# Kernel optimization log

Measured on AMD Instinct MI355X. Metric: run time of the kernel, lower is better.

Reference implementation:

```python
import jax, jax.numpy as jnp
import numpy as np

HEAD_DIM = 128
NUM_Q_HEADS = 32
NUM_KV_HEADS = 8
ROPE_BASE = 500000.0
# llama3 rope scaling constants
OLD_CTX = 8192.0
SCALE_FACTOR = 8.0
LOW_FREQ_FACTOR = 1.0
HIGH_FREQ_FACTOR = 4.0


def _llama3_inv_freq(dim):
    inv_freq = ROPE_BASE ** (-jnp.arange(0, dim, 2, dtype=jnp.float32) / dim)
    wavelen = 2.0 * jnp.pi / inv_freq
    low_wl = OLD_CTX / LOW_FREQ_FACTOR
    high_wl = OLD_CTX / HIGH_FREQ_FACTOR
    smooth = (OLD_CTX / wavelen - LOW_FREQ_FACTOR) / (HIGH_FREQ_FACTOR - LOW_FREQ_FACTOR)
    smoothed = (1.0 - smooth) * inv_freq / SCALE_FACTOR + smooth * inv_freq
    return jnp.where(wavelen > low_wl, inv_freq / SCALE_FACTOR,
                     jnp.where(wavelen < high_wl, inv_freq, smoothed))


def _apply_rope(x, cos, sin):
    # x: [B,N,H,D]; cos/sin: [B,N,1,D/2]  (NeoX rotate-half convention)
    x1, x2 = jnp.split(x, 2, axis=-1)
    return jnp.concatenate([x1 * cos - x2 * sin, x2 * cos + x1 * sin], axis=-1)


def setup_inputs() -> dict:
    key = jax.random.key(0)
    k1, k2, k3 = jax.random.split(key, 3)
    B, N, H = 2, 2048, 4096
    qkv_out = (NUM_Q_HEADS + 2 * NUM_KV_HEADS) * HEAD_DIM  # 6144
    x = jax.random.normal(k1, (B, N, H), dtype=jnp.float32)
    positions = jnp.tile(jnp.arange(N, dtype=jnp.int32), (B, 1))
    wqkv = jax.random.normal(k2, (H, qkv_out), dtype=jnp.float32) * 0.02
    wo = jax.random.normal(k3, (NUM_Q_HEADS * HEAD_DIM, H), dtype=jnp.float32) * 0.02
    return {"x": x, "positions": positions, "wqkv": wqkv, "wo": wo}


def reference(x, positions, wqkv, wo):
    B, N, H = x.shape
    q_size = NUM_Q_HEADS * HEAD_DIM
    kv_size = NUM_KV_HEADS * HEAD_DIM
    # fused QKV projection
    qkv = jnp.einsum('bnh,hd->bnd', x, wqkv)
    q, k, v = jnp.split(qkv, [q_size, q_size + kv_size], axis=-1)
    q = q.reshape(B, N, NUM_Q_HEADS, HEAD_DIM)
    k = k.reshape(B, N, NUM_KV_HEADS, HEAD_DIM)
    v = v.reshape(B, N, NUM_KV_HEADS, HEAD_DIM)
    # llama3-scaled RoPE
    inv_freq = _llama3_inv_freq(HEAD_DIM)  # [D/2]
    freqs = positions[..., None].astype(jnp.float32) * inv_freq  # [B,N,D/2]
    cos = jnp.cos(freqs)[:, :, None, :]
    sin = jnp.sin(freqs)[:, :, None, :]
    q = _apply_rope(q, cos, sin)
    k = _apply_rope(k, cos, sin)
    # GQA causal attention
    g = NUM_Q_HEADS // NUM_KV_HEADS
    qg = q.reshape(B, N, NUM_KV_HEADS, g, HEAD_DIM)
    scale = 1.0 / np.sqrt(HEAD_DIM).astype(np.float32)
    scores = jnp.einsum('bnkgd,bmkd->bkgnm', qg, k) * scale  # [B,KV,G,N,N]
    causal = jnp.tril(jnp.ones((N, N), dtype=bool))
    scores = jnp.where(causal, scores, jnp.finfo(scores.dtype).min)
    p = jax.nn.softmax(scores, axis=-1)
    o = jnp.einsum('bkgnm,bmkd->bnkgd', p, v).reshape(B, N, NUM_Q_HEADS * HEAD_DIM)
    return jnp.einsum('bnd,dh->bnh', o, wo)
```

## Files before the change

### kernel.cpp

```cpp
#include <hip/hip_runtime.h>
#include <math.h>

typedef float  floatx4 __attribute__((ext_vector_type(4)));
typedef short  shortx8 __attribute__((ext_vector_type(8)));
typedef __bf16 bf16x8  __attribute__((ext_vector_type(8)));

static __device__ __forceinline__ floatx4 mfma16(shortx8 a, shortx8 b, floatx4 c) {
  return __builtin_amdgcn_mfma_f32_16x16x32_bf16(
      __builtin_bit_cast(bf16x8, a), __builtin_bit_cast(bf16x8, b), c, 0, 0, 0);
}
static __device__ __forceinline__ unsigned short f2bf(float f) {
  unsigned int u = __builtin_bit_cast(unsigned int, f);
  u += 0x7fffu + ((u >> 16) & 1u);
  return (unsigned short)(u >> 16);
}
static __device__ __forceinline__ float bf2f(unsigned short h) {
  unsigned int u = ((unsigned int)h) << 16;
  return __builtin_bit_cast(float, u);
}
static __device__ __forceinline__ unsigned int packbf2(float lo, float hi) {
  return (unsigned int)f2bf(lo) | ((unsigned int)f2bf(hi) << 16);
}

#define GLOAD_LDS16(gp, lp) \
  __builtin_amdgcn_global_load_lds((const __attribute__((address_space(1))) void*)(gp), \
                                   (__attribute__((address_space(3))) void*)(lp), 16, 0, 0)

__global__ __launch_bounds__(256) void conv_kernel(const float* __restrict__ in,
                                                   unsigned short* __restrict__ out, long n4) {
  long i = (long)blockIdx.x * 256 + threadIdx.x;
  if (i < n4) {
    float4 v = ((const float4*)in)[i];
    uint2 st;
    st.x = packbf2(v.x, v.y);
    st.y = packbf2(v.z, v.w);
    ((uint2*)out)[i] = st;
  }
}

__global__ __launch_bounds__(256) void tconv_kernel(const float* __restrict__ in,
                                                    unsigned short* __restrict__ out,
                                                    int R, int C) {
  __shared__ float t[32][33];
  const int r0 = blockIdx.x * 32, c0 = blockIdx.y * 32;
  const int tr = threadIdx.x >> 3, tq = threadIdx.x & 7;
  float4 v = *(const float4*)(in + (long)(r0 + tr) * C + c0 + tq * 4);
  t[tr][tq * 4 + 0] = v.x;
  t[tr][tq * 4 + 1] = v.y;
  t[tr][tq * 4 + 2] = v.z;
  t[tr][tq * 4 + 3] = v.w;
  __syncthreads();
  const int cl = tr, rq = tq;
  uint2 st;
  st.x = packbf2(t[rq * 4 + 0][cl], t[rq * 4 + 1][cl]);
  st.y = packbf2(t[rq * 4 + 2][cl], t[rq * 4 + 3][cl]);
  *(uint2*)(out + (long)(c0 + cl) * R + r0 + rq * 4) = st;
}

template<int C_BF16>
__global__ __launch_bounds__(256) void gemm_tt(const unsigned short* __restrict__ A,
                                               const unsigned short* __restrict__ BT,
                                               void* __restrict__ Cp,
                                               int Nn, int K, int lda) {
  __shared__ alignas(16) short As[128 * 32];
  __shared__ alignas(16) short Bs[128 * 32];
  const int tid = threadIdx.x;
  const int lane = tid & 63, w = tid >> 6;
  const int l15 = lane & 15, lg = lane >> 4;
  const int wr = w >> 1, wc = w & 1;
  const int klg = lg ^ ((l15 >> 1) & 3);
  const long m0 = (long)blockIdx.x * 128;
  const long n0 = (long)blockIdx.y * 128;

  floatx4 acc[4][4];
#pragma unroll
  for (int m = 0; m < 4; ++m)
#pragma unroll
    for (int n = 0; n < 4; ++n) acc[m][n] = (floatx4)0.0f;

  for (int k0 = 0; k0 < K; k0 += 32) {
#pragma unroll
    for (int i = 0; i < 2; ++i) {
      int c = i * 256 + tid;
      int row = c >> 2, j = c & 3;
      int kc = j ^ ((row >> 1) & 3);
      const unsigned short* ga = A + (m0 + row) * (long)lda + k0 + kc * 8;
      GLOAD_LDS16(ga, (char*)As + i * 4096 + w * 1024);
      const unsigned short* gb = BT + (n0 + row) * (long)K + k0 + kc * 8;
      GLOAD_LDS16(gb, (char*)Bs + i * 4096 + w * 1024);
    }
    __syncthreads();

    shortx8 afr[4], bfr[4];
#pragma unroll
    for (int m = 0; m < 4; ++m)
      afr[m] = *(const shortx8*)((char*)As + (wr * 64 + m * 16 + l15) * 64 + klg * 16);
#pragma unroll
    for (int n = 0; n < 4; ++n)
      bfr[n] = *(const shortx8*)((char*)Bs + (wc * 64 + n * 16 + l15) * 64 + klg * 16);
#pragma unroll
    for (int m = 0; m < 4; ++m)
#pragma unroll
      for (int n = 0; n < 4; ++n)
        acc[m][n] = mfma16(afr[m], bfr[n], acc[m][n]);
    __syncthreads();
  }

#pragma unroll
  for (int m = 0; m < 4; ++m)
#pragma unroll
    for (int n = 0; n < 4; ++n)
#pragma unroll
      for (int r = 0; r < 4; ++r) {
        long row = m0 + wr * 64 + m * 16 + lg * 4 + r;
        long col = n0 + wc * 64 + n * 16 + l15;
        float val = acc[m][n][r];
        if constexpr (C_BF16) ((unsigned short*)Cp)[row * Nn + col] = f2bf(val);
        else                  ((float*)Cp)[row * Nn + col] = val;
      }
}

template<int A_BF16, int C_BF16>
__global__ __launch_bounds__(256) void gemm_fb(const void* __restrict__ Ap,
                                               const float* __restrict__ Bp,
                                               void* __restrict__ Cp,
                                               int M, int Nn, int K, int lda) {
  __shared__ alignas(16) short As[128 * 40];
  __shared__ alignas(16) short Bs[128 * 40];
  const int tid = threadIdx.x;
  const int lane = tid & 63, w = tid >> 6;
  const int l15 = lane & 15, lg = lane >> 4;
  const int wr = w >> 1, wc = w & 1;
  const long m0 = (long)blockIdx.x * 128;
  const long n0 = (long)blockIdx.y * 128;

  floatx4 acc[4][4];
#pragma unroll
  for (int m = 0; m < 4; ++m)
#pragma unroll
    for (int n = 0; n < 4; ++n) acc[m][n] = (floatx4)0.0f;

  for (int k0 = 0; k0 < K; k0 += 32) {
    if constexpr (A_BF16) {
      const unsigned short* A = (const unsigned short*)Ap;
#pragma unroll
      for (int i = 0; i < 2; ++i) {
        int qi = tid + 256 * i;
        int row = qi >> 2, ch = qi & 3;
        uint4 v = *(const uint4*)(A + (m0 + row) * (long)lda + k0 + ch * 8);
        *(uint4*)((char*)As + row * 80 + ch * 16) = v;
      }
    } else {
      const float* A = (const float*)Ap;
#pragma unroll
      for (int i = 0; i < 4; ++i) {
        int qi = tid + 256 * i;
        int row = qi >> 3, q = qi & 7;
        float4 v = *(const float4*)(A + (m0 + row) * (long)lda + k0 + q * 4);
        uint2 st;
        st.x = packbf2(v.x, v.y);
        st.y = packbf2(v.z, v.w);
        *(uint2*)((char*)As + row * 80 + q * 8) = st;
      }
    }
#pragma unroll
    for (int i = 0; i < 2; ++i) {
      int qi = tid + 256 * i;
      int kp = qi >> 5, q = qi & 31;
      const float* B0 = Bp + (long)(k0 + 2 * kp) * Nn + n0 + q * 4;
      float4 a = *(const float4*)B0;
      float4 b = *(const float4*)(B0 + Nn);
      const float* af_ = (const float*)&a;
      const float* bf_ = (const float*)&b;
#pragma unroll
      for (int j = 0; j < 4; ++j) {
        int col = q * 4 + j;
        *(unsigned int*)((char*)Bs + col * 80 + kp * 4) = packbf2(af_[j], bf_[j]);
      }
    }
    __syncthreads();

    shortx8 afr[4], bfr[4];
#pragma unroll
    for (int m = 0; m < 4; ++m)
      afr[m] = *(const shortx8*)((char*)As + (wr * 64 + m * 16 + l15) * 80 + lg * 16);
#pragma unroll
    for (int n = 0; n < 4; ++n)
      bfr[n] = *(const shortx8*)((char*)Bs + (wc * 64 + n * 16 + l15) * 80 + lg * 16);
#pragma unroll
    for (int m = 0; m < 4; ++m)
#pragma unroll
      for (int n = 0; n < 4; ++n)
        acc[m][n] = mfma16(afr[m], bfr[n], acc[m][n]);
    __syncthreads();
  }

#pragma unroll
  for (int m = 0; m < 4; ++m)
#pragma unroll
    for (int n = 0; n < 4; ++n)
#pragma unroll
      for (int r = 0; r < 4; ++r) {
        long row = m0 + wr * 64 + m * 16 + lg * 4 + r;
        long col = n0 + wc * 64 + n * 16 + l15;
        float val = acc[m][n][r];
        if constexpr (C_BF16) ((unsigned short*)Cp)[row * Nn + col] = f2bf(val);
        else                  ((float*)Cp)[row * Nn + col] = val;
      }
}

__global__ __launch_bounds__(256) void rope_kernel(unsigned short* __restrict__ qkv,
                                                   const int* __restrict__ pos) {
  const int token = blockIdx.x;
  const int tid = threadIdx.x;
  __shared__ float cs[64], sn[64];
  if (tid < 64) {
    float d = (float)tid;
    float inv = powf(500000.0f, -d * (1.0f / 64.0f));
    float wl = 6.283185307179586f / inv;
    float scaled;
    if (wl > 8192.0f) scaled = inv * 0.125f;
    else if (wl < 2048.0f) scaled = inv;
    else {
      float smooth = (8192.0f / wl - 1.0f) * (1.0f / 3.0f);
      scaled = (1.0f - smooth) * inv * 0.125f + smooth * inv;
    }
    float ang = (float)pos[token] * scaled;
    cs[tid] = cosf(ang);
    sn[tid] = sinf(ang);
  }
  __syncthreads();
  const long base = (long)token * 6144;
#pragma unroll
  for (int it = 0; it < 10; ++it) {
    int p = tid + 256 * it;
    int h = p >> 6, d = p & 63;
    long i0 = base + h * 128 + d;
    float a = bf2f(qkv[i0]);
    float b = bf2f(qkv[i0 + 64]);
    float c = cs[d], s = sn[d];
    qkv[i0]      = f2bf(a * c - b * s);
    qkv[i0 + 64] = f2bf(b * c + a * s);
  }
}

#define SCALE_QK 0.08838834764831845f
__global__ __launch_bounds__(256) void attn_kernel(unsigned short* __restrict__ qkv) {
  const int tid = threadIdx.x;
  const int w = tid >> 6, lane = tid & 63;
  const int l15 = lane & 15, lg = lane >> 4;
  const int qblk = blockIdx.x, qh = blockIdx.y, b = blockIdx.z;
  const int kvh = qh >> 2;
  const int q0 = qblk * 64;
  const long rowbase = (long)b * 2048;

  __shared__ alignas(16) short Ks[64 * 128];
  __shared__ alignas(16) short Vt[128 * 64];
  __shared__ alignas(16) short Ps[4][16 * 64];

  shortx8 qf[4];
  {
    long qrow = rowbase + q0 + w * 16 + l15;
    const unsigned short* qp = qkv + qrow * 6144 + qh * 128 + lg * 8;
#pragma unroll
    for (int dc = 0; dc < 4; ++dc) qf[dc] = *(const shortx8*)(qp + dc * 32);
  }

  floatx4 accO[8];
#pragma unroll
  for (int i = 0; i < 8; ++i) accO[i] = (floatx4)0.0f;
  float m_r[4], l_r[4];
#pragma unroll
  for (int r = 0; r < 4; ++r) { m_r[r] = -INFINITY; l_r[r] = 0.0f; }

  const int nt = qblk + 1;
  for (int t = 0; t < nt; ++t) {
    const int kt0 = t * 64;
#pragma unroll
    for (int i = 0; i < 4; ++i) {
      int ci = tid + 256 * i;
      int tok = ci >> 4, ch = ci & 15;
      uint4 v = *(const uint4*)(qkv + (rowbase + kt0 + tok) * 6144 + 4096 + kvh * 128 + ch * 8);
      int byte = (tok * 256 + ch * 16) ^ ((tok & 7) << 4);
      *(uint4*)((char*)Ks + byte) = v;
    }
#pragma unroll
    for (int i = 0; i < 4; ++i) {
      int ci = tid + 256 * i;
      int tok = ci >> 4, ch = ci & 15;
      uint4 v = *(const uint4*)(qkv + (rowbase + kt0 + tok) * 6144 + 5120 + kvh * 128 + ch * 8);
      const unsigned short* e = (const unsigned short*)&v;
#pragma unroll
      for (int j = 0; j < 8; ++j) {
        int d = ch * 8 + j;
        int byte = (d * 128 + tok * 2) ^ (((d ^ (d >> 3)) & 7) << 4);
        *(short*)((char*)Vt + byte) = (short)e[j];
      }
    }
    __syncthreads();

    floatx4 accS[4];
#pragma unroll
    for (int c = 0; c < 4; ++c) accS[c] = (floatx4)0.0f;
#pragma unroll
    for (int c = 0; c < 4; ++c) {
      int tok = c * 16 + l15;
      int rb = tok * 256, sw = (tok & 7) << 4;
#pragma unroll
      for (int dc = 0; dc < 4; ++dc) {
        shortx8 kf = *(const shortx8*)((char*)Ks + ((rb + dc * 64 + lg * 16) ^ sw));
        accS[c] = mfma16(qf[dc], kf, accS[c]);
      }
    }

    float sv[4][4], rm[4];
    const int growb = q0 + w * 16 + lg * 4;
    const bool diag = (t == nt - 1);
#pragma unroll
    for (int r = 0; r < 4; ++r) rm[r] = -INFINITY;
#pragma unroll
    for (int c = 0; c < 4; ++c) {
      int gcol = kt0 + c * 16 + l15;
#pragma unroll
      for (int r = 0; r < 4; ++r) {
        float s = accS[c][r] * SCALE_QK;
        if (diag && gcol > growb + r) s = -1e30f;
        sv[c][r] = s;
        rm[r] = fmaxf(rm[r], s);
      }
    }
#pragma unroll
    for (int r = 0; r < 4; ++r) {
      rm[r] = fmaxf(rm[r], __shfl_xor(rm[r], 1));
      rm[r] = fmaxf(rm[r], __shfl_xor(rm[r], 2));
      rm[r] = fmaxf(rm[r], __shfl_xor(rm[r], 4));
      rm[r] = fmaxf(rm[r], __shfl_xor(rm[r], 8));
    }
    float alpha[4], rs[4], mn[4];
#pragma unroll
    for (int r = 0; r < 4; ++r) {
      mn[r] = fmaxf(m_r[r], rm[r]);
      alpha[r] = __expf(m_r[r] - mn[r]);
      rs[r] = 0.0f;
    }
    char* Pw = (char*)&Ps[w][0];
#pragma unroll
    for (int c = 0; c < 4; ++c) {
#pragma unroll
      for (int r = 0; r < 4; ++r) {
        float p = __expf(sv[c][r] - mn[r]);
        rs[r] += p;
        int row = lg * 4 + r, col = c * 16 + l15;
        int byte = (row * 128 + col * 2) ^ ((row & 7) << 4);
        *(short*)(Pw + byte) = (short)f2bf(p);
      }
    }
#pragma unroll
    for (int r = 0; r < 4; ++r) {
      rs[r] += __shfl_xor(rs[r], 1);
      rs[r] += __shfl_xor(rs[r], 2);
      rs[r] += __shfl_xor(rs[r], 4);
      rs[r] += __shfl_xor(rs[r], 8);
      l_r[r] = l_r[r] * alpha[r] + rs[r];
      m_r[r] = mn[r];
    }
#pragma unroll
    for (int db = 0; db < 8; ++db)
#pragma unroll
      for (int r = 0; r < 4; ++r) accO[db][r] *= alpha[r];

#pragma unroll
    for (int kc = 0; kc < 2; ++kc) {
      int pb = (l15 * 128 + kc * 64 + lg * 16) ^ ((l15 & 7) << 4);
      shortx8 pf = *(const shortx8*)(Pw + pb);
#pragma unroll
      for (int db = 0; db < 8; ++db) {
        int d = db * 16 + l15;
        int vb = (d * 128 + kc * 64 + lg * 16) ^ (((d ^ (d >> 3)) & 7) << 4);
        shortx8 vf = *(const shortx8*)((char*)Vt + vb);
        accO[db] = mfma16(pf, vf, accO[db]);
      }
    }
    __syncthreads();
  }

  {
    long orow_base = rowbase + q0 + w * 16 + lg * 4;
#pragma unroll
    for (int r = 0; r < 4; ++r) {
      float inv_l = 1.0f / l_r[r];
      unsigned short* op = qkv + (orow_base + r) * 6144 + qh * 128 + l15;
#pragma unroll
      for (int db = 0; db < 8; ++db) op[db * 16] = f2bf(accO[db][r] * inv_l);
    }
  }
}

extern "C" void kernel_launch(void* const* d_in, const int* in_sizes, int n_in,
                              void* d_out, int out_size, void* d_ws, size_t ws_size,
                              hipStream_t stream) {
  const float* x    = (const float*)d_in[0];
  const int*   posi = (const int*)d_in[1];
  const float* wqkv = (const float*)d_in[2];
  const float* wo   = (const float*)d_in[3];
  float* out = (float*)d_out;
  unsigned short* qkv = (unsigned short*)d_ws;

  const size_t off_wqT = 50331648;
  const size_t off_xb  = off_wqT + 50331648;
  const size_t need    = off_xb + 33554432;

  if (ws_size >= need) {
    unsigned short* wqT = (unsigned short*)((char*)d_ws + off_wqT);
    unsigned short* xb  = (unsigned short*)((char*)d_ws + off_xb);
    unsigned short* woT = xb;

    conv_kernel<<<dim3(16384), 256, 0, stream>>>(x, xb, 4194304);
    tconv_kernel<<<dim3(128, 192), 256, 0, stream>>>(wqkv, wqT, 4096, 6144);
    gemm_tt<1><<<dim3(32, 48), 256, 0, stream>>>(xb, wqT, (void*)qkv, 6144, 4096, 4096);
    rope_kernel<<<dim3(4096), 256, 0, stream>>>(qkv, posi);
    tconv_kernel<<<dim3(128, 128), 256, 0, stream>>>(wo, woT, 4096, 4096);
    attn_kernel<<<dim3(32, 32, 2), 256, 0, stream>>>(qkv);
    gemm_tt<0><<<dim3(32, 32), 256, 0, stream>>>(qkv, woT, (void*)out, 4096, 4096, 6144);
  } else {
    gemm_fb<0, 1><<<dim3(32, 48), 256, 0, stream>>>(
        (const void*)x, wqkv, (void*)qkv, 4096, 6144, 4096, 4096);
    rope_kernel<<<dim3(4096), 256, 0, stream>>>(qkv, posi);
    attn_kernel<<<dim3(32, 32, 2), 256, 0, stream>>>(qkv);
    gemm_fb<1, 0><<<dim3(32, 32), 256, 0, stream>>>(
        (const void*)qkv, wo, (void*)out, 4096, 4096, 4096, 6144);
  }
}
```

Measured before the change: 1.296 ms.

## Share K/V tiles across GQA query heads per attention block with reversed scheduling

Restructures the attention kernel so each block serves one KV head. Its four warps each handle a different query head of the group over 32 query rows, so each loaded K/V tile is reused by four heads instead of one. Blocks are issued in reverse order so the longest causal rows start first. The V transpose into shared memory now packs two tokens per 32-bit store. The change cuts redundant global K/V loads and shared-memory staging per query row, but doubles per-warp register state (two row-groups of accumulators) and enlarges the P buffer, which may lower occupancy.

New measurement: 1.177 ms. -9.2%, faster.

```diff
diff --git a/kernel.cpp b/kernel.cpp
--- a/kernel.cpp
+++ b/kernel.cpp
@@ -249,31 +249,39 @@
   const int tid = threadIdx.x;
   const int w = tid >> 6, lane = tid & 63;
   const int l15 = lane & 15, lg = lane >> 4;
-  const int qblk = blockIdx.x, qh = blockIdx.y, b = blockIdx.z;
-  const int kvh = qh >> 2;
-  const int q0 = qblk * 64;
+  const int s = 63 - blockIdx.x;
+  const int kvh = blockIdx.y, b = blockIdx.z;
+  const int h = kvh * 4 + w;
+  const int q0 = s * 32;
   const long rowbase = (long)b * 2048;
 
   __shared__ alignas(16) short Ks[64 * 128];
   __shared__ alignas(16) short Vt[128 * 64];
-  __shared__ alignas(16) short Ps[4][16 * 64];
-
-  shortx8 qf[4];
-  {
-    long qrow = rowbase + q0 + w * 16 + l15;
-    const unsigned short* qp = qkv + qrow * 6144 + qh * 128 + lg * 8;
-#pragma unroll
-    for (int dc = 0; dc < 4; ++dc) qf[dc] = *(const shortx8*)(qp + dc * 32);
-  }
-
-  floatx4 accO[8];
-#pragma unroll
-  for (int i = 0; i < 8; ++i) accO[i] = (floatx4)0.0f;
-  float m_r[4], l_r[4];
-#pragma unroll
-  for (int r = 0; r < 4; ++r) { m_r[r] = -INFINITY; l_r[r] = 0.0f; }
-
-  const int nt = qblk + 1;
+  __shared__ alignas(16) short Ps[4][32 * 64];
+
+  shortx8 qf[2][4];
+#pragma unroll
+  for (int m = 0; m < 2; ++m) {
+    long qrow = rowbase + q0 + m * 16 + l15;
+    const unsigned short* qp = qkv + qrow * 6144 + h * 128 + lg * 8;
+#pragma unroll
+    for (int dc = 0; dc < 4; ++dc) qf[m][dc] = *(const shortx8*)(qp + dc * 32);
+  }
+
+  floatx4 accO[2][8];
+#pragma unroll
+  for (int m = 0; m < 2; ++m)
+#pragma unroll
+    for (int i = 0; i < 8; ++i) accO[m][i] = (floatx4)0.0f;
+  float m_r[2][4], l_r[2][4];
+#pragma unroll
+  for (int m = 0; m < 2; ++m)
+#pragma unroll
+    for (int r = 0; r < 4; ++r) { m_r[m][r] = -INFINITY; l_r[m][r] = 0.0f; }
+
+  const int nt = (s >> 1) + 1;
+  char* Pw = (char*)&Ps[w][0];
+
   for (int t = 0; t < nt; ++t) {
     const int kt0 = t * 64;
 #pragma unroll
@@ -285,113 +293,120 @@
       *(uint4*)((char*)Ks + byte) = v;
     }
 #pragma unroll
-    for (int i = 0; i < 4; ++i) {
-      int ci = tid + 256 * i;
-      int tok = ci >> 4, ch = ci & 15;
-      uint4 v = *(const uint4*)(qkv + (rowbase + kt0 + tok) * 6144 + 5120 + kvh * 128 + ch * 8);
-      const unsigned short* e = (const unsigned short*)&v;
+    for (int i = 0; i < 2; ++i) {
+      int pu = tid + 256 * i;
+      int tp = pu >> 4, ch = pu & 15;
+      const unsigned short* vrow = qkv + (rowbase + kt0 + 2 * tp) * 6144 + 5120 + kvh * 128 + ch * 8;
+      uint4 a = *(const uint4*)(vrow);
+      uint4 c2 = *(const uint4*)(vrow + 6144);
+      const unsigned short* ea = (const unsigned short*)&a;
+      const unsigned short* eb = (const unsigned short*)&c2;
 #pragma unroll
       for (int j = 0; j < 8; ++j) {
         int d = ch * 8 + j;
-        int byte = (d * 128 + tok * 2) ^ (((d ^ (d >> 3)) & 7) << 4);
-        *(short*)((char*)Vt + byte) = (short)e[j];
-      }
-    }
-    __syncthreads();
-
-    floatx4 accS[4];
-#pragma unroll
-    for (int c = 0; c < 4; ++c) accS[c] = (floatx4)0.0f;
-#pragma unroll
-    for (int c = 0; c < 4; ++c) {
-      int tok = c * 16 + l15;
-      int rb = tok * 256, sw = (tok & 7) << 4;
-#pragma unroll
-      for (int dc = 0; dc < 4; ++dc) {
-        shortx8 kf = *(const shortx8*)((char*)Ks + ((rb + dc * 64 + lg * 16) ^ sw));
-        accS[c] = mfma16(qf[dc], kf, accS[c]);
-      }
-    }
-
-    float sv[4][4], rm[4];
-    const int growb = q0 + w * 16 + lg * 4;
+        int byte = (d * 128 + tp * 4) ^ (((d ^ (d >> 3)) & 7) << 4);
+        *(unsigned int*)((char*)Vt + byte) = (unsigned int)ea[j] | ((unsigned int)eb[j] << 16);
+      }
+    }
+    __syncthreads();
+
     const bool diag = (t == nt - 1);
 #pragma unroll
-    for (int r = 0; r < 4; ++r) rm[r] = -INFINITY;
-#pragma unroll
-    for (int c = 0; c < 4; ++c) {
-      int gcol = kt0 + c * 16 + l15;
+    for (int m = 0; m < 2; ++m) {
+      floatx4 accS[4];
+#pragma unroll
+      for (int c = 0; c < 4; ++c) accS[c] = (floatx4)0.0f;
+#pragma unroll
+      for (int c = 0; c < 4; ++c) {
+        int tok = c * 16 + l15;
+        int rb = tok * 256, sw = (tok & 7) << 4;
+#pragma unroll
+        for (int dc = 0; dc < 4; ++dc) {
+          shortx8 kf = *(const shortx8*)((char*)Ks + ((rb + dc * 64 + lg * 16) ^ sw));
+          accS[c] = mfma16(qf[m][dc], kf, accS[c]);
+        }
+      }
+
+      float sv[4][4], rm[4];
+      const int growb = q0 + m * 16 + lg * 4;
+#pragma unroll
+      for (int r = 0; r < 4; ++r) rm[r] = -INFINITY;
+#pragma unroll
+      for (int c = 0; c < 4; ++c) {
+        int gcol = kt0 + c * 16 + l15;
+#pragma unroll
+        for (int r = 0; r < 4; ++r) {
+          float sc = accS[c][r] * SCALE_QK;
+          if (diag && gcol > growb + r) sc = -1e30f;
+          sv[c][r] = sc;
+          rm[r] = fmaxf(rm[r], sc);
+        }
+      }
 #pragma unroll
       for (int r = 0; r < 4; ++r) {
-        float s = accS[c][r] * SCALE_QK;
-        if (diag && gcol > growb + r) s = -1e30f;
-        sv[c][r] = s;
-        rm[r] = fmaxf(rm[r], s);
-      }
-    }
+        rm[r] = fmaxf(rm[r], __shfl_xor(rm[r], 1));
+        rm[r] = fmaxf(rm[r], __shfl_xor(rm[r], 2));
+        rm[r] = fmaxf(rm[r], __shfl_xor(rm[r], 4));
+        rm[r] = fmaxf(rm[r], __shfl_xor(rm[r], 8));
+      }
+      float alpha[4], rs[4], mn[4];
+#pragma unroll
+      for (int r = 0; r < 4; ++r) {
+        mn[r] = fmaxf(m_r[m][r], rm[r]);
+        alpha[r] = __expf(m_r[m][r] - mn[r]);
+        rs[r] = 0.0f;
+      }
+#pragma unroll
+      for (int c = 0; c < 4; ++c) {
+#pragma unroll
+        for (int r = 0; r < 4; ++r) {
+          float p = __expf(sv[c][r] - mn[r]);
+          rs[r] += p;
+          int row = m * 16 + lg * 4 + r, col = c * 16 + l15;
+          int byte = (row * 128 + col * 2) ^ ((row & 7) << 4);
+          *(short*)(Pw + byte) = (short)f2bf(p);
+        }
+      }
+#pragma unroll
+      for (int r = 0; r < 4; ++r) {
+        rs[r] += __shfl_xor(rs[r], 1);
+        rs[r] += __shfl_xor(rs[r], 2);
+        rs[r] += __shfl_xor(rs[r], 4);
+        rs[r] += __shfl_xor(rs[r], 8);
+        l_r[m][r] = l_r[m][r] * alpha[r] + rs[r];
+        m_r[m][r] = mn[r];
+      }
+#pragma unroll
+      for (int db = 0; db < 8; ++db)
+#pragma unroll
+        for (int r = 0; r < 4; ++r) accO[m][db][r] *= alpha[r];
+
+#pragma unroll
+      for (int kc = 0; kc < 2; ++kc) {
+        int prow = m * 16 + l15;
+        int pb = (prow * 128 + kc * 64 + lg * 16) ^ ((l15 & 7) << 4);
+        shortx8 pf = *(const shortx8*)(Pw + pb);
+#pragma unroll
+        for (int db = 0; db < 8; ++db) {
+          int d = db * 16 + l15;
+          int vb = (d * 128 + kc * 64 + lg * 16) ^ (((d ^ (d >> 3)) & 7) << 4);
+          shortx8 vf = *(const shortx8*)((char*)Vt + vb);
+          accO[m][db] = mfma16(pf, vf, accO[m][db]);
+        }
+      }
+    }
+    __syncthreads();
+  }
+
+#pragma unroll
+  for (int m = 0; m < 2; ++m) {
+    long orow_base = rowbase + q0 + m * 16 + lg * 4;
 #pragma unroll
     for (int r = 0; r < 4; ++r) {
-      rm[r] = fmaxf(rm[r], __shfl_xor(rm[r], 1));
-      rm[r] = fmaxf(rm[r], __shfl_xor(rm[r], 2));
-      rm[r] = fmaxf(rm[r], __shfl_xor(rm[r], 4));
-      rm[r] = fmaxf(rm[r], __shfl_xor(rm[r], 8));
-    }
-    float alpha[4], rs[4], mn[4];
-#pragma unroll
-    for (int r = 0; r < 4; ++r) {
-      mn[r] = fmaxf(m_r[r], rm[r]);
-      alpha[r] = __expf(m_r[r] - mn[r]);
-      rs[r] = 0.0f;
-    }
-    char* Pw = (char*)&Ps[w][0];
-#pragma unroll
-    for (int c = 0; c < 4; ++c) {
-#pragma unroll
-      for (int r = 0; r < 4; ++r) {
-        float p = __expf(sv[c][r] - mn[r]);
-        rs[r] += p;
-        int row = lg * 4 + r, col = c * 16 + l15;
-        int byte = (row * 128 + col * 2) ^ ((row & 7) << 4);
-        *(short*)(Pw + byte) = (short)f2bf(p);
-      }
-    }
-#pragma unroll
-    for (int r = 0; r < 4; ++r) {
-      rs[r] += __shfl_xor(rs[r], 1);
-      rs[r] += __shfl_xor(rs[r], 2);
-      rs[r] += __shfl_xor(rs[r], 4);
-      rs[r] += __shfl_xor(rs[r], 8);
-      l_r[r] = l_r[r] * alpha[r] + rs[r];
-      m_r[r] = mn[r];
-    }
-#pragma unroll
-    for (int db = 0; db < 8; ++db)
-#pragma unroll
-      for (int r = 0; r < 4; ++r) accO[db][r] *= alpha[r];
-
-#pragma unroll
-    for (int kc = 0; kc < 2; ++kc) {
-      int pb = (l15 * 128 + kc * 64 + lg * 16) ^ ((l15 & 7) << 4);
-      shortx8 pf = *(const shortx8*)(Pw + pb);
-#pragma unroll
-      for (int db = 0; db < 8; ++db) {
-        int d = db * 16 + l15;
-        int vb = (d * 128 + kc * 64 + lg * 16) ^ (((d ^ (d >> 3)) & 7) << 4);
-        shortx8 vf = *(const shortx8*)((char*)Vt + vb);
-        accO[db] = mfma16(pf, vf, accO[db]);
-      }
-    }
-    __syncthreads();
-  }
-
-  {
-    long orow_base = rowbase + q0 + w * 16 + lg * 4;
-#pragma unroll
-    for (int r = 0; r < 4; ++r) {
-      float inv_l = 1.0f / l_r[r];
-      unsigned short* op = qkv + (orow_base + r) * 6144 + qh * 128 + l15;
-#pragma unroll
-      for (int db = 0; db < 8; ++db) op[db * 16] = f2bf(accO[db][r] * inv_l);
+      float inv_l = 1.0f / l_r[m][r];
+      unsigned short* op = qkv + (orow_base + r) * 6144 + h * 128 + l15;
+#pragma unroll
+      for (int db = 0; db < 8; ++db) op[db * 16] = f2bf(accO[m][db][r] * inv_l);
     }
   }
 }
@@ -420,13 +435,13 @@
     gemm_tt<1><<<dim3(32, 48), 256, 0, stream>>>(xb, wqT, (void*)qkv, 6144, 4096, 4096);
     rope_kernel<<<dim3(4096), 256, 0, stream>>>(qkv, posi);
     tconv_kernel<<<dim3(128, 128), 256, 0, stream>>>(wo, woT, 4096, 4096);
-    attn_kernel<<<dim3(32, 32, 2), 256, 0, stream>>>(qkv);
+    attn_kernel<<<dim3(64, 8, 2), 256, 0, stream>>>(qkv);
     gemm_tt<0><<<dim3(32, 32), 256, 0, stream>>>(qkv, woT, (void*)out, 4096, 4096, 6144);
   } else {
     gemm_fb<0, 1><<<dim3(32, 48), 256, 0, stream>>>(
         (const void*)x, wqkv, (void*)qkv, 4096, 6144, 4096, 4096);
     rope_kernel<<<dim3(4096), 256, 0, stream>>>(qkv, posi);
-    attn_kernel<<<dim3(32, 32, 2), 256, 0, stream>>>(qkv);
+    attn_kernel<<<dim3(64, 8, 2), 256, 0, stream>>>(qkv);
     gemm_fb<1, 0><<<dim3(32, 32), 256, 0, stream>>>(
         (const void*)qkv, wo, (void*)out, 4096, 4096, 4096, 6144);
   }
```
